# Kernel tuning notes

Measured on AMD Instinct MI355X. Metric: run time of the kernel, lower is better.

Reference implementation:

```python
import jax, jax.numpy as jnp
import numpy as np

B, G, D, H = 8, 32, 768, 12
N = G * G
HD = D // H  # 64


def _make_rope(grid_size, head_dim):
    half = head_dim // 2
    inv_freq = 1.0 / (10000.0 ** (jnp.arange(0, half, 2, dtype=jnp.float32) / half))  # [half//2]
    pos = jnp.arange(grid_size, dtype=jnp.float32)[:, None] * inv_freq[None, :]       # [G, half//2]
    emb1 = jnp.concatenate([jnp.sin(pos), jnp.cos(pos)], axis=-1)                     # [G, half]
    emb_x = jnp.broadcast_to(emb1[None, :, :], (grid_size, grid_size, half))          # vary along x
    emb_y = jnp.broadcast_to(emb1[:, None, :], (grid_size, grid_size, half))          # vary along y
    emb = jnp.concatenate([emb_y, emb_x], axis=-1).reshape(grid_size * grid_size, head_dim)
    cos = jnp.cos(emb).reshape(1, grid_size * grid_size, 1, head_dim)
    sin = jnp.sin(emb).reshape(1, grid_size * grid_size, 1, head_dim)
    return cos, sin


def setup_inputs() -> dict:
    key = jax.random.key(0)
    kx, kw1, kb1, kw2, kb2 = jax.random.split(key, 5)
    x = jax.random.normal(kx, (B, N, D), dtype=jnp.float32)
    qkv_w = jax.random.normal(kw1, (3 * D, D), dtype=jnp.float32) * 0.02
    qkv_b = jax.random.normal(kb1, (3 * D,), dtype=jnp.float32) * 0.02
    proj_w = jax.random.normal(kw2, (D, D), dtype=jnp.float32) * 0.02
    proj_b = jax.random.normal(kb2, (D,), dtype=jnp.float32) * 0.02
    cos_emb, sin_emb = _make_rope(G, HD)
    return {"x": x, "qkv_w": qkv_w, "qkv_b": qkv_b, "proj_w": proj_w,
            "proj_b": proj_b, "cos_emb": cos_emb, "sin_emb": sin_emb}


def _apply_rope(t, cos, sin):
    # t: [B, N, H, HD]; cos/sin: [1, N, 1, HD]
    t1, t2 = t[..., 0::2], t[..., 1::2]
    rotated = jnp.concatenate([-t2, t1], axis=-1)
    return t * cos + rotated * sin


def reference(x, qkv_w, qkv_b, proj_w, proj_b, cos_emb, sin_emb):
    b, n, d = x.shape
    qkv = (x @ qkv_w.T + qkv_b).reshape(b, n, 3, H, HD)
    q, k, v = qkv[:, :, 0], qkv[:, :, 1], qkv[:, :, 2]  # [B, N, H, HD]
    q = _apply_rope(q, cos_emb, sin_emb)
    k = _apply_rope(k, cos_emb, sin_emb)
    scale = HD ** -0.5
    attn = jnp.einsum('bnhd,bmhd->bhnm', q, k) * scale
    attn = jax.nn.softmax(attn, axis=-1)
    out = jnp.einsum('bhnm,bmhd->bnhd', attn, v).reshape(b, n, d)
    return out @ proj_w.T + proj_b
```

## Files before the change

kernel.cpp:

```cpp
#include <hip/hip_runtime.h>
#include <stdint.h>
#include <stddef.h>

#define B_    8
#define NPOS  1024
#define DMODEL 768
#define NHEAD 12
#define HDIM  64
#define MTOK  (B_*NPOS)

typedef short bf16x8 __attribute__((ext_vector_type(8)));
typedef float f32x4  __attribute__((ext_vector_type(4)));

#if __has_builtin(__builtin_amdgcn_exp2f)
#define EXP2(x) __builtin_amdgcn_exp2f(x)
#else
#define EXP2(x) exp2f(x)
#endif

__device__ __forceinline__ unsigned short f2bs(float f) {
    unsigned int u = __builtin_bit_cast(unsigned int, f);
    u += 0x7FFFu + ((u >> 16) & 1u);
    return (unsigned short)(u >> 16);
}
__device__ __forceinline__ unsigned short f2bs_fast(float f) {
    unsigned int u = __builtin_bit_cast(unsigned int, f);
    return (unsigned short)((u + 0x8000u) >> 16);
}
__device__ __forceinline__ float bs2f(unsigned short s) {
    unsigned int u = ((unsigned int)s) << 16;
    return __builtin_bit_cast(float, u);
}

template<int N> __device__ __forceinline__ void vwait() {
    asm volatile("s_waitcnt vmcnt(%0)" :: "n"(N) : "memory");
}

__device__ __forceinline__ void gload16(const void* g, void* l) {
    __builtin_amdgcn_global_load_lds(
        (const __attribute__((address_space(1))) unsigned int*)g,
        (__attribute__((address_space(3))) unsigned int*)l, 16, 0, 0);
}

__global__ void cvt_all(const float* __restrict__ x, const float* __restrict__ w1,
                        const float* __restrict__ w2,
                        unsigned short* __restrict__ xb, unsigned short* __restrict__ wb,
                        unsigned short* __restrict__ pwb)
{
    const int N0 = MTOK * DMODEL / 4;
    const int N1 = 3 * DMODEL * DMODEL / 4;
    const int N2 = DMODEL * DMODEL / 4;
    int i = blockIdx.x * blockDim.x + threadIdx.x;
    int stride = gridDim.x * blockDim.x;
    for (; i < N0 + N1 + N2; i += stride) {
        const float4* s; unsigned short* d; int k;
        if (i < N0)            { s = (const float4*)x;  d = xb;  k = i; }
        else if (i < N0 + N1)  { s = (const float4*)w1; d = wb;  k = i - N0; }
        else                   { s = (const float4*)w2; d = pwb; k = i - N0 - N1; }
        float4 v = s[k];
        ushort4 o; o.x = f2bs(v.x); o.y = f2bs(v.y); o.z = f2bs(v.z); o.w = f2bs(v.w);
        ((ushort4*)d)[k] = o;
    }
}

__global__ __launch_bounds__(256)
void qkv_gemm_rope(const unsigned short* __restrict__ xb, const unsigned short* __restrict__ wb,
                   const float* __restrict__ bias, const float* __restrict__ cosE,
                   const float* __restrict__ sinE,
                   unsigned short* __restrict__ qb, unsigned short* __restrict__ kbuf,
                   unsigned short* __restrict__ vt)
{
    __shared__ char smem[65536];
    char* As0 = smem;
    char* Bs0 = smem + 16384;
    char* As1 = smem + 32768;
    char* Bs1 = smem + 49152;
    float* ct = (float*)smem;

    const int tid = threadIdx.x;
    const int lane = tid & 63, w = tid >> 6;
    const int wr = w >> 1, wc = w & 1;

    const int bid = blockIdx.x;
    const int xcd = bid & 7, idx = bid >> 3;
    const int n0 = (idx % 18) * 128;
    const int m0 = (xcd * 8 + idx / 18) * 128;

    const char* aS[4]; const char* bS[4]; int sDo[4];
    #pragma unroll
    for (int j = 0; j < 4; j++) {
        int i   = w * 4 + j;
        int row = i * 8 + (lane >> 3);
        int kb  = ((lane & 7) << 4) ^ ((row & 7) << 4);
        aS[j] = (const char*)(xb + (size_t)(m0 + row) * DMODEL) + kb;
        bS[j] = (const char*)(wb + (size_t)(n0 + row) * DMODEL) + kb;
        sDo[j] = i * 1024;
    }
    int aOf[2][4], bOf[2][4];
    #pragma unroll
    for (int kc = 0; kc < 2; kc++) {
        int chunk = kc * 4 + (lane >> 4);
        #pragma unroll
        for (int f = 0; f < 4; f++) {
            int ra = wr*64 + f*16 + (lane & 15);
            aOf[kc][f] = ra*128 + ((chunk << 4) ^ ((ra & 7) << 4));
            int rb = wc*64 + f*16 + (lane & 15);
            bOf[kc][f] = rb*128 + ((chunk << 4) ^ ((rb & 7) << 4));
        }
    }

    f32x4 acc[4][4];
    #pragma unroll
    for (int i = 0; i < 4; i++)
        #pragma unroll
        for (int j = 0; j < 4; j++) acc[i][j] = (f32x4){0.f, 0.f, 0.f, 0.f};

    auto gcompute = [&](char* Ac, char* Bc) {
        #pragma unroll
        for (int kc = 0; kc < 2; kc++) {
            bf16x8 af[4], bfr[4];
            #pragma unroll
            for (int mf = 0; mf < 4; mf++) af[mf] = *(const bf16x8*)(Ac + aOf[kc][mf]);
            #pragma unroll
            for (int nf = 0; nf < 4; nf++) bfr[nf] = *(const bf16x8*)(Bc + bOf[kc][nf]);
            #pragma unroll
            for (int mf = 0; mf < 4; mf++)
                #pragma unroll
                for (int nf = 0; nf < 4; nf++)
                    acc[mf][nf] = __builtin_amdgcn_mfma_f32_16x16x32_bf16(af[mf], bfr[nf], acc[mf][nf], 0, 0, 0);
        }
    };

#define QSTAGE(KOFF, AB, BB) do { \
    _Pragma("unroll") for (int j = 0; j < 4; j++) gload16(aS[j] + (KOFF), (AB) + sDo[j]); \
    _Pragma("unroll") for (int j = 0; j < 4; j++) gload16(bS[j] + (KOFF), (BB) + sDo[j]); \
} while (0)

    QSTAGE(0,   As0, Bs0);
    QSTAGE(128, As1, Bs1);

#define QSTEP(T, AC, BC, VM) \
    vwait<VM>(); \
    __builtin_amdgcn_s_barrier(); \
    gcompute(AC, BC); \
    __builtin_amdgcn_s_barrier(); \
    if ((T) + 2 < 12) QSTAGE(((T) + 2) * 128, AC, BC);

#define QPAIR(T, VM1) QSTEP(T, As0, Bs0, 8) QSTEP((T)+1, As1, Bs1, VM1)
    QPAIR(0, 8) QPAIR(2, 8) QPAIR(4, 8) QPAIR(6, 8) QPAIR(8, 8) QPAIR(10, 0)
#undef QPAIR
#undef QSTEP
#undef QSTAGE

    const int s  = n0 / DMODEL;
    const int h2 = (n0 % DMODEL) / 64;
    #pragma unroll
    for (int p = 0; p < 2; p++) {
        if (wr == p) {
            #pragma unroll
            for (int mf = 0; mf < 4; mf++)
                #pragma unroll
                for (int nf = 0; nf < 4; nf++) {
                    int c = wc*64 + nf*16 + (lane & 15);
                    float bv = bias[n0 + c];
                    #pragma unroll
                    for (int reg = 0; reg < 4; reg++) {
                        int r = mf*16 + ((lane >> 4) << 2) + reg;
                        ct[r*130 + c] = acc[mf][nf][reg] + bv;
                    }
                }
        }
        __syncthreads();
        const int rowg = m0 + p*64;
        const int bb   = rowg >> 10;
        const int pos0 = rowg & 1023;
        if (s < 2) {
            unsigned short* dst = (s == 0) ? qb : kbuf;
            const float qs = (s == 0) ? 0.125f * 1.44269504f : 1.0f;
            const int d = tid & 63, r0 = tid >> 6;
            for (int r = r0; r < 64; r += 4) {
                int pos = pos0 + r;
                float cv = cosE[pos*64 + d] * qs, sv = sinE[pos*64 + d] * qs;
                #pragma unroll
                for (int hh = 0; hh < 2; hh++) {
                    const float* rowp = ct + r*130 + hh*64;
                    float val = rowp[d];
                    float rot = (d < 32) ? -rowp[2*d + 1] : rowp[2*d - 64];
                    dst[(((size_t)(bb*NHEAD + h2 + hh))*NPOS + pos)*64 + d] = f2bs(val*cv + rot*sv);
                }
            }
        } else {
            const int posi = tid & 63, c0 = tid >> 6;
            for (int cc = c0; cc < 128; cc += 4) {
                int hh = cc >> 6, d = cc & 63;
                vt[(((size_t)(bb*NHEAD + h2 + hh))*64 + d)*NPOS + pos0 + posi] =
                    f2bs(ct[posi*130 + cc]);
            }
        }
        __syncthreads();
    }
}

__global__ __launch_bounds__(256)
void attn_mfma(const unsigned short* __restrict__ qb, const unsigned short* __restrict__ kbuf,
               const unsigned short* __restrict__ vt,
               unsigned short* __restrict__ att)
{
    __shared__ char smem[49152];
    char* Kb0 = smem;
    char* Kb1 = smem + 8192;
    char* Vb0 = smem + 16384;
    char* Vb1 = smem + 24576;
    char* Pq  = smem + 32768;

    const int tid = threadIdx.x;
    const int lane = tid & 63, w = tid >> 6;
    char* Pw = Pq + w * 4096;

    const int bid = blockIdx.x;
    const int swz = (bid & 7) * 96 + (bid >> 3);
    const int bh = swz >> 3, qt = swz & 7;
    const int bb = bh / NHEAD, hh = bh % NHEAD;
    const int q0 = qt * 128;

    const unsigned short* qp = qb   + (size_t)bh * NPOS * 64;
    const unsigned short* kp = kbuf + (size_t)bh * NPOS * 64;
    const unsigned short* vp = vt   + (size_t)bh * 64 * NPOS;

    const char* kS[2]; const char* vS[2]; int kvDo[2];
    #pragma unroll
    for (int j = 0; j < 2; j++) {
        int i   = w * 2 + j;
        int row = i * 8 + (lane >> 3);
        int kb  = ((lane & 7) << 4) ^ ((row & 7) << 4);
        kS[j] = (const char*)(kp) + (size_t)row * 128 + kb;
        vS[j] = (const char*)(vp) + (size_t)row * 2048 + kb;
        kvDo[j] = i * 1024;
    }
    int kOf[2][4], vOf[2][4], pOf[2][2];
    #pragma unroll
    for (int kc = 0; kc < 2; kc++) {
        int chunk = kc * 4 + (lane >> 4);
        #pragma unroll
        for (int f = 0; f < 4; f++) {
            int r = f*16 + (lane & 15);
            kOf[kc][f] = r*128 + ((chunk << 4) ^ ((r & 7) << 4));
            vOf[kc][f] = kOf[kc][f];
        }
        #pragma unroll
        for (int f = 0; f < 2; f++) {
            int r = f*16 + (lane & 15);
            pOf[kc][f] = r*128 + ((chunk << 4) ^ ((r & 7) << 4));
        }
    }

#define ASTAGE(T, KN, VN) do { \
    _Pragma("unroll") for (int j = 0; j < 2; j++) gload16(kS[j] + (size_t)(T) * 8192, (KN) + kvDo[j]); \
    _Pragma("unroll") for (int j = 0; j < 2; j++) gload16(vS[j] + (T) * 128,          (VN) + kvDo[j]); \
} while (0)

    #pragma unroll
    for (int j = 0; j < 4; j++) {
        int i   = w * 4 + j;
        int row = i * 8 + (lane >> 3);
        int kb  = ((lane & 7) << 4) ^ ((row & 7) << 4);
        gload16((const char*)(qp + (size_t)(q0 + row) * 64) + kb, Pq + i * 1024);
    }
    ASTAGE(0, Kb0, Vb0);
    vwait<4>();
    __builtin_amdgcn_s_barrier();
    bf16x8 qf[2][2];
    #pragma unroll
    for (int mf = 0; mf < 2; mf++)
        #pragma unroll
        for (int kc = 0; kc < 2; kc++)
            qf[mf][kc] = *(const bf16x8*)(Pq + w*4096 + pOf[kc][mf]);

    f32x4 O[2][4];
    float lpart[2][4];
    #pragma unroll
    for (int mf = 0; mf < 2; mf++)
        #pragma unroll
        for (int nd = 0; nd < 4; nd++) O[mf][nd] = (f32x4){0.f, 0.f, 0.f, 0.f};
    #pragma unroll
    for (int mf = 0; mf < 2; mf++)
        #pragma unroll
        for (int reg = 0; reg < 4; reg++) lpart[mf][reg] = 0.f;

    auto abody = [&](char* Kc, char* Vc) {
        f32x4 S[2][4];
        #pragma unroll
        for (int mf = 0; mf < 2; mf++)
            #pragma unroll
            for (int nf = 0; nf < 4; nf++) S[mf][nf] = (f32x4){0.f, 0.f, 0.f, 0.f};
        #pragma unroll
        for (int kc = 0; kc < 2; kc++) {
            bf16x8 kf[4];
            #pragma unroll
            for (int nf = 0; nf < 4; nf++) kf[nf] = *(const bf16x8*)(Kc + kOf[kc][nf]);
            __builtin_amdgcn_s_setprio(1);
            #pragma unroll
            for (int mf = 0; mf < 2; mf++)
                #pragma unroll
                for (int nf = 0; nf < 4; nf++)
                    S[mf][nf] = __builtin_amdgcn_mfma_f32_16x16x32_bf16(qf[mf][kc], kf[nf], S[mf][nf], 0, 0, 0);
            __builtin_amdgcn_s_setprio(0);
        }
        #pragma unroll
        for (int mf = 0; mf < 2; mf++) {
            #pragma unroll
            for (int reg = 0; reg < 4; reg++) {
                int ql = mf*16 + ((lane >> 4) << 2) + reg;
                #pragma unroll
                for (int nf = 0; nf < 4; nf++) {
                    float pv = EXP2(S[mf][nf][reg]);
                    lpart[mf][reg] += pv;
                    int key = nf*16 + (lane & 15);
                    *(unsigned short*)(Pw + ql*128 + ((key*2) ^ ((ql & 7) << 4))) = f2bs_fast(pv);
                }
            }
        }
        #pragma unroll
        for (int kc = 0; kc < 2; kc++) {
            bf16x8 pf[2], vf[4];
            #pragma unroll
            for (int mf = 0; mf < 2; mf++) pf[mf] = *(const bf16x8*)(Pw + pOf[kc][mf]);
            #pragma unroll
            for (int nd = 0; nd < 4; nd++) vf[nd] = *(const bf16x8*)(Vc + vOf[kc][nd]);
            __builtin_amdgcn_s_setprio(1);
            #pragma unroll
            for (int mf = 0; mf < 2; mf++)
                #pragma unroll
                for (int nd = 0; nd < 4; nd++)
                    O[mf][nd] = __builtin_amdgcn_mfma_f32_16x16x32_bf16(pf[mf], vf[nd], O[mf][nd], 0, 0, 0);
            __builtin_amdgcn_s_setprio(0);
        }
    };

#define ASTEP(T, KC, VC, KN, VN, VM) \
    if ((T) + 1 < 16) ASTAGE((T) + 1, KN, VN); \
    vwait<VM>(); \
    __builtin_amdgcn_s_barrier(); \
    abody(KC, VC); \
    __builtin_amdgcn_s_barrier();

#define APAIR(T, VM1) ASTEP(T, Kb0, Vb0, Kb1, Vb1, 4) ASTEP((T)+1, Kb1, Vb1, Kb0, Vb0, VM1)
    APAIR(0, 4) APAIR(2, 4) APAIR(4, 4) APAIR(6, 4)
    APAIR(8, 4) APAIR(10, 4) APAIR(12, 4) APAIR(14, 0)
#undef APAIR
#undef ASTEP
#undef ASTAGE

    #pragma unroll
    for (int mf = 0; mf < 2; mf++)
        #pragma unroll
        for (int reg = 0; reg < 4; reg++) {
            float l = lpart[mf][reg];
            l += __shfl_xor(l, 1);
            l += __shfl_xor(l, 2);
            l += __shfl_xor(l, 4);
            l += __shfl_xor(l, 8);
            float inv = 1.f / l;
            int qg = q0 + w*32 + mf*16 + ((lane >> 4) << 2) + reg;
            size_t rowb = ((size_t)bb * NPOS + qg) * DMODEL + hh * 64;
            #pragma unroll
            for (int nd = 0; nd < 4; nd++) {
                int d = nd*16 + (lane & 15);
                att[rowb + d] = f2bs(O[mf][nd][reg] * inv);
            }
        }
}

__global__ __launch_bounds__(256)
void proj_gemm(const unsigned short* __restrict__ a, const unsigned short* __restrict__ wgt,
               const float* __restrict__ bias, float* __restrict__ out)
{
    __shared__ char smem[65536];
    char* As0 = smem;
    char* Bs0 = smem + 16384;
    char* As1 = smem + 32768;
    char* Bs1 = smem + 49152;

    const int tid = threadIdx.x;
    const int lane = tid & 63, w = tid >> 6;
    const int wr = w >> 1, wc = w & 1;

    const int bid = blockIdx.x;
    const int xcd = bid & 7, idx = bid >> 3;
    const int n0 = (idx % 6) * 128;
    const int m0 = (xcd * 8 + idx / 6) * 128;

    const char* aS[4]; const char* bS[4]; int sDo[4];
    #pragma unroll
    for (int j = 0; j < 4; j++) {
        int i   = w * 4 + j;
        int row = i * 8 + (lane >> 3);
        int kb  = ((lane & 7) << 4) ^ ((row & 7) << 4);
        aS[j] = (const char*)(a   + (size_t)(m0 + row) * DMODEL) + kb;
        bS[j] = (const char*)(wgt + (size_t)(n0 + row) * DMODEL) + kb;
        sDo[j] = i * 1024;
    }
    int aOf[2][4], bOf[2][4];
    #pragma unroll
    for (int kc = 0; kc < 2; kc++) {
        int chunk = kc * 4 + (lane >> 4);
        #pragma unroll
        for (int f = 0; f < 4; f++) {
            int ra = wr*64 + f*16 + (lane & 15);
            aOf[kc][f] = ra*128 + ((chunk << 4) ^ ((ra & 7) << 4));
            int rb = wc*64 + f*16 + (lane & 15);
            bOf[kc][f] = rb*128 + ((chunk << 4) ^ ((rb & 7) << 4));
        }
    }

    f32x4 acc[4][4];
    #pragma unroll
    for (int i = 0; i < 4; i++)
        #pragma unroll
        for (int j = 0; j < 4; j++) acc[i][j] = (f32x4){0.f, 0.f, 0.f, 0.f};

    auto gcompute = [&](char* Ac, char* Bc) {
        #pragma unroll
        for (int kc = 0; kc < 2; kc++) {
            bf16x8 af[4], bfr[4];
            #pragma unroll
            for (int mf = 0; mf < 4; mf++) af[mf] = *(const bf16x8*)(Ac + aOf[kc][mf]);
            #pragma unroll
            for (int nf = 0; nf < 4; nf++) bfr[nf] = *(const bf16x8*)(Bc + bOf[kc][nf]);
            #pragma unroll
            for (int mf = 0; mf < 4; mf++)
                #pragma unroll
                for (int nf = 0; nf < 4; nf++)
                    acc[mf][nf] = __builtin_amdgcn_mfma_f32_16x16x32_bf16(af[mf], bfr[nf], acc[mf][nf], 0, 0, 0);
        }
    };

#define PSTAGE(KOFF, AB, BB) do { \
    _Pragma("unroll") for (int j = 0; j < 4; j++) gload16(aS[j] + (KOFF), (AB) + sDo[j]); \
    _Pragma("unroll") for (int j = 0; j < 4; j++) gload16(bS[j] + (KOFF), (BB) + sDo[j]); \
} while (0)

    PSTAGE(0,   As0, Bs0);
    PSTAGE(128, As1, Bs1);

#define PSTEP(T, AC, BC, VM) \
    vwait<VM>(); \
    __builtin_amdgcn_s_barrier(); \
    gcompute(AC, BC); \
    __builtin_amdgcn_s_barrier(); \
    if ((T) + 2 < 12) PSTAGE(((T) + 2) * 128, AC, BC);

#define PPAIR(T, VM1) PSTEP(T, As0, Bs0, 8) PSTEP((T)+1, As1, Bs1, VM1)
    PPAIR(0, 8) PPAIR(2, 8) PPAIR(4, 8) PPAIR(6, 8) PPAIR(8, 8) PPAIR(10, 0)
#undef PPAIR
#undef PSTEP
#undef PSTAGE

    #pragma unroll
    for (int mf = 0; mf < 4; mf++)
        #pragma unroll
        for (int nf = 0; nf < 4; nf++) {
            int c = n0 + wc*64 + nf*16 + (lane & 15);
            float bv = bias[c];
            #pragma unroll
            for (int reg = 0; reg < 4; reg++) {
                int r = m0 + wr*64 + mf*16 + ((lane >> 4) << 2) + reg;
                out[(size_t)r * DMODEL + c] = acc[mf][nf][reg] + bv;
            }
        }
}

extern "C" void kernel_launch(void* const* d_in, const int* in_sizes, int n_in,
                              void* d_out, int out_size, void* d_ws, size_t ws_size,
                              hipStream_t stream)
{
    (void)in_sizes; (void)n_in; (void)out_size; (void)ws_size;
    const float* x      = (const float*)d_in[0];
    const float* qkv_w  = (const float*)d_in[1];
    const float* qkv_b  = (const float*)d_in[2];
    const float* proj_w = (const float*)d_in[3];
    const float* proj_b = (const float*)d_in[4];
    const float* cosE   = (const float*)d_in[5];
    const float* sinE   = (const float*)d_in[6];
    float* out = (float*)d_out;

    char* ws = (char*)d_ws;
    unsigned short* xb  = (unsigned short*)(ws);
    unsigned short* wb  = (unsigned short*)(ws + 12582912);
    unsigned short* pwb = (unsigned short*)(ws + 16121856);
    unsigned short* qb  = (unsigned short*)(ws + 17301504);
    unsigned short* kbf = (unsigned short*)(ws + 29884416);
    unsigned short* vtp = (unsigned short*)(ws + 42467328);
    unsigned short* att = (unsigned short*)(ws + 55050240);

    cvt_all<<<2048, 256, 0, stream>>>(x, qkv_w, proj_w, xb, wb, pwb);
    qkv_gemm_rope<<<1152, 256, 0, stream>>>(xb, wb, qkv_b, cosE, sinE, qb, kbf, vtp);
    attn_mfma<<<768, 256, 0, stream>>>(qb, kbf, vtp, att);
    proj_gemm<<<384, 256, 0, stream>>>(att, pwb, proj_b, out);
}
```

Measured before the change: 120.9 us.

## Triple-buffer A tiles in QKV GEMM to issue A loads before compute

The QKV GEMM mainloop now uses three A buffers and two B buffers. The next A tile is issued right after the barrier, before the MFMA compute, while B is still loaded after compute. This is meant to give A loads more time to overlap with math. LDS grows from 64KB to 80KB, which may reduce occupancy. The attention kernel also drops a duplicate V offset array and reuses the K offsets, which saves registers.

```diff
diff --git a/kernel.cpp b/kernel.cpp
--- a/kernel.cpp
+++ b/kernel.cpp
@@ -70,11 +70,12 @@
                    unsigned short* __restrict__ qb, unsigned short* __restrict__ kbuf,
                    unsigned short* __restrict__ vt)
 {
-    __shared__ char smem[65536];
-    char* As0 = smem;
-    char* Bs0 = smem + 16384;
-    char* As1 = smem + 32768;
-    char* Bs1 = smem + 49152;
+    __shared__ char smem[81920];
+    char* Ab0 = smem;
+    char* Ab1 = smem + 16384;
+    char* Ab2 = smem + 32768;
+    char* Bb0 = smem + 49152;
+    char* Bb1 = smem + 65536;
     float* ct = (float*)smem;
 
     const int tid = threadIdx.x;
@@ -131,26 +132,39 @@
         }
     };
 
-#define QSTAGE(KOFF, AB, BB) do { \
-    _Pragma("unroll") for (int j = 0; j < 4; j++) gload16(aS[j] + (KOFF), (AB) + sDo[j]); \
-    _Pragma("unroll") for (int j = 0; j < 4; j++) gload16(bS[j] + (KOFF), (BB) + sDo[j]); \
+#define ASTG(T, AB) do { \
+    _Pragma("unroll") for (int j = 0; j < 4; j++) gload16(aS[j] + (T) * 128, (AB) + sDo[j]); \
 } while (0)
-
-    QSTAGE(0,   As0, Bs0);
-    QSTAGE(128, As1, Bs1);
-
-#define QSTEP(T, AC, BC, VM) \
+#define BSTG(T, BB) do { \
+    _Pragma("unroll") for (int j = 0; j < 4; j++) gload16(bS[j] + (T) * 128, (BB) + sDo[j]); \
+} while (0)
+
+    ASTG(0, Ab0); BSTG(0, Bb0);
+    ASTG(1, Ab1); BSTG(1, Bb1);
+
+#define QSTEP(T, AC, BC, AN, VM) \
     vwait<VM>(); \
     __builtin_amdgcn_s_barrier(); \
+    if ((T) + 2 < 12) ASTG((T) + 2, AN); \
     gcompute(AC, BC); \
     __builtin_amdgcn_s_barrier(); \
-    if ((T) + 2 < 12) QSTAGE(((T) + 2) * 128, AC, BC);
-
-#define QPAIR(T, VM1) QSTEP(T, As0, Bs0, 8) QSTEP((T)+1, As1, Bs1, VM1)
-    QPAIR(0, 8) QPAIR(2, 8) QPAIR(4, 8) QPAIR(6, 8) QPAIR(8, 8) QPAIR(10, 0)
-#undef QPAIR
+    if ((T) + 2 < 12) BSTG((T) + 2, BC);
+
+    QSTEP(0,  Ab0, Bb0, Ab2, 8)
+    QSTEP(1,  Ab1, Bb1, Ab0, 8)
+    QSTEP(2,  Ab2, Bb0, Ab1, 8)
+    QSTEP(3,  Ab0, Bb1, Ab2, 8)
+    QSTEP(4,  Ab1, Bb0, Ab0, 8)
+    QSTEP(5,  Ab2, Bb1, Ab1, 8)
+    QSTEP(6,  Ab0, Bb0, Ab2, 8)
+    QSTEP(7,  Ab1, Bb1, Ab0, 8)
+    QSTEP(8,  Ab2, Bb0, Ab1, 8)
+    QSTEP(9,  Ab0, Bb1, Ab2, 8)
+    QSTEP(10, Ab1, Bb0, Ab0, 8)
+    QSTEP(11, Ab2, Bb1, Ab0, 0)
 #undef QSTEP
-#undef QSTAGE
+#undef ASTG
+#undef BSTG
 
     const int s  = n0 / DMODEL;
     const int h2 = (n0 % DMODEL) / 64;
@@ -237,7 +251,7 @@
         vS[j] = (const char*)(vp) + (size_t)row * 2048 + kb;
         kvDo[j] = i * 1024;
     }
-    int kOf[2][4], vOf[2][4], pOf[2][2];
+    int kOf[2][4], pOf[2][2];
     #pragma unroll
     for (int kc = 0; kc < 2; kc++) {
         int chunk = kc * 4 + (lane >> 4);
@@ -245,7 +259,6 @@
         for (int f = 0; f < 4; f++) {
             int r = f*16 + (lane & 15);
             kOf[kc][f] = r*128 + ((chunk << 4) ^ ((r & 7) << 4));
-            vOf[kc][f] = kOf[kc][f];
         }
         #pragma unroll
         for (int f = 0; f < 2; f++) {
@@ -326,7 +339,7 @@
             #pragma unroll
             for (int mf = 0; mf < 2; mf++) pf[mf] = *(const bf16x8*)(Pw + pOf[kc][mf]);
             #pragma unroll
-            for (int nd = 0; nd < 4; nd++) vf[nd] = *(const bf16x8*)(Vc + vOf[kc][nd]);
+            for (int nd = 0; nd < 4; nd++) vf[nd] = *(const bf16x8*)(Vc + kOf[kc][nd]);
             __builtin_amdgcn_s_setprio(1);
             #pragma unroll
             for (int mf = 0; mf < 2; mf++)
```

Measured after the change: 120.6 us (median of 2 runs). No clear change (-0.2%).
